# Optimization experiments

Hardware: AMD Instinct MI355X
Metric: run time of the kernel (lower is better)

Reference implementation:

```python
import jax, jax.numpy as jnp
import numpy as np

# ---- static config (from init_kwargs) ----
N = 500_000            # total points
B = 4                  # batch size (lidar frames)
VX, VY, VZ = 0.2, 0.2, 4.0
PC = (0.0, -40.0, -3.0, 70.4, 40.0, 1.0)  # point cloud range
NZ = int((PC[5] - PC[2]) / VZ)   # 1
NY = int((PC[4] - PC[1]) / VY)   # 400
NX = int((PC[3] - PC[0]) / VX)   # 352
CANVAS = B * NZ * NY * NX        # dense voxel canvas (563200)
EPS = 1e-3                       # BN eps
XOFF = VX / 2 + PC[0]
YOFF = VY / 2 + PC[1]
ZOFF = VZ / 2 + PC[2]
C0, C1 = 64, 128                 # feat_channels
CIN = 13                         # 4 + 2(spatial) + 3(cluster) + 3(center) + 1(dist)


def setup_inputs() -> dict:
    key = jax.random.key(0)
    ks = jax.random.split(key, 12)
    # points uniformly in the point-cloud range, plus intensity
    xyz = jax.random.uniform(ks[0], (N, 3), dtype=jnp.float32) \
        * jnp.array([70.4, 80.0, 4.0], jnp.float32) \
        + jnp.array([0.0, -40.0, -3.0], jnp.float32)
    inten = jax.random.uniform(ks[1], (N, 1), dtype=jnp.float32)
    features = jnp.concatenate([xyz, inten], axis=1)  # (N, 4)
    # voxel coords consistent with the points; batch idx sorted so coors[-1,0]==B-1
    bidx = jnp.sort(jax.random.randint(ks[2], (N,), 0, B, dtype=jnp.int32))
    zc = jnp.clip(((xyz[:, 2] - PC[2]) / VZ).astype(jnp.int32), 0, NZ - 1)
    yc = jnp.clip(((xyz[:, 1] - PC[1]) / VY).astype(jnp.int32), 0, NY - 1)
    xc = jnp.clip(((xyz[:, 0] - PC[0]) / VX).astype(jnp.int32), 0, NX - 1)
    coors = jnp.stack([bidx, zc, yc, xc], axis=1)  # (N, 4) [b, z, y, x]
    # VFE weights (Linear bias=False) + BN affine params
    s0 = 1.0 / np.sqrt(CIN)
    s1 = 1.0 / np.sqrt(2 * C0)
    s2 = 1.0 / np.sqrt(C1 + 2)
    W0 = jax.random.uniform(ks[3], (CIN, C0), jnp.float32, -s0, s0)
    g0 = jnp.ones((C0,), jnp.float32)
    b0 = jnp.zeros((C0,), jnp.float32)
    W1 = jax.random.uniform(ks[4], (2 * C0, C1), jnp.float32, -s1, s1)
    g1 = jnp.ones((C1,), jnp.float32)
    b1 = jnp.zeros((C1,), jnp.float32)
    Ws = jax.random.uniform(ks[5], (C1 + 2, C1), jnp.float32, -s2, s2)
    bs = jax.random.uniform(ks[6], (C1,), jnp.float32, -s2, s2)
    return {"features": features, "coors": coors,
            "W0": W0, "g0": g0, "b0": b0,
            "W1": W1, "g1": g1, "b1": b1,
            "Ws": Ws, "bs": bs}


def _bn_relu(x, g, b):
    # BN1d in training mode: batch statistics (biased var), eps=1e-3
    m = jnp.mean(x, axis=0)
    v = jnp.var(x, axis=0)
    return jax.nn.relu((x - m) * jax.lax.rsqrt(v + EPS) * g + b)


def reference(features, coors, W0, g0, b0, W1, g1, b1, Ws, bs):
    xyz = features[:, :3]
    # linear voxel id on the dense canvas: b*Z*Y*X + z*Y*X + y*X + x
    v = ((coors[:, 0] * NZ + coors[:, 1]) * NY + coors[:, 2]) * NX + coors[:, 3]
    v = v.astype(jnp.int32)

    # ---- calculate_spatial_features (unique + index_add -> segment reductions) ----
    counts = jax.ops.segment_sum(jnp.ones((N,), features.dtype), v, CANVAS)
    safe = jnp.maximum(counts, 1.0)                       # clamp(min=1)
    density = safe / (VX * VY * VZ)                       # per-voxel point density
    sum_coords = jax.ops.segment_sum(xyz, v, CANVAS)      # (CANVAS, 3)
    voxel_mean = sum_coords / safe[:, None]
    point_mean = voxel_mean[v]                            # gather back to points
    pdist = jnp.linalg.norm(xyz - point_mean, axis=1)
    mean_dist = (jax.ops.segment_sum(pdist, v, CANVAS) / safe)[v]
    f_spatial = jnp.stack([density[v], mean_dist], axis=1)  # (N, 2)

    # ---- cluster center (avg scatter + gather): same voxel mean ----
    f_cluster = xyz - point_mean                          # (N, 3)

    # ---- voxel center offsets ----
    cf = coors.astype(features.dtype)
    f_center = jnp.stack([
        xyz[:, 0] - (cf[:, 3] * VX + XOFF),
        xyz[:, 1] - (cf[:, 2] * VY + YOFF),
        xyz[:, 2] - (cf[:, 1] * VZ + ZOFF)], axis=1)      # (N, 3)

    # ---- distance ----
    f_dist = jnp.linalg.norm(xyz, axis=1, keepdims=True)  # (N, 1)

    x = jnp.concatenate([features, f_spatial, f_cluster, f_center, f_dist], axis=1)  # (N, 13)

    # ---- VFE layer 0: Linear -> BN -> ReLU, scatter-max, gather, concat ----
    p = _bn_relu(x @ W0, g0, b0)                          # (N, 64)
    vmax = jax.ops.segment_max(p, v, CANVAS)              # (CANVAS, 64), -inf on empty
    x = jnp.concatenate([p, vmax[v]], axis=1)             # (N, 128)

    # ---- VFE layer 1 + feature_scaling ----
    p = _bn_relu(x @ W1, g1, b1)                          # (N, 128)
    p = jax.nn.relu(jnp.concatenate([p, f_spatial], axis=1) @ Ws + bs)  # (N, 128)
    return p  # return_point_feats=True
```

## Files before the change

### kernel.cpp

```cpp
#include <hip/hip_runtime.h>
#include <hip/hip_bf16.h>

#define NZv 1
#define NYv 400
#define NXv 352
#define Bv 4
#define CANVASv (Bv * NZv * NYv * NXv)
#define EPSF 0.001f
#define VXF 0.2f
#define VYF 0.2f
#define VZF 4.0f
#define XOFFv 0.1f
#define YOFFv -39.9f
#define ZOFFv -1.0f

typedef __attribute__((ext_vector_type(8))) short bf16x8;
typedef __attribute__((ext_vector_type(4))) float f32x4;
typedef __attribute__((ext_vector_type(2))) unsigned int u32x2;

__device__ __forceinline__ short f2bf(float f) {
    union { __hip_bfloat16 h; short s; } u;
    u.h = __float2bfloat16(f);
    return u.s;
}
__device__ __forceinline__ float bf2f(short s) {
    return __uint_as_float(((unsigned int)(unsigned short)s) << 16);
}
__device__ __forceinline__ unsigned int pk(float a, float b) {
    return (unsigned int)(unsigned short)f2bf(a) | ((unsigned int)(unsigned short)f2bf(b) << 16);
}

struct MomTab { signed char a[105]; signed char b[105]; };
constexpr MomTab make_momtab() {
    MomTab m{};
    int idx = 0;
    for (int a = 0; a < 14; ++a)
        for (int b = a; b < 14; ++b) { m.a[idx] = (signed char)a; m.b[idx] = (signed char)b; ++idx; }
    return m;
}
constexpr MomTab MT = make_momtab();

__global__ void k_scatter1(const int4* __restrict__ coors, int* __restrict__ vidx,
                           float* __restrict__ counts, int n)
{
    int i = blockIdx.x * blockDim.x + threadIdx.x;
    if (i >= n) return;
    int4 c = coors[i];
    int v = ((c.x * NZv + c.y) * NYv + c.z) * NXv + c.w;
    vidx[i] = v;
    atomicAdd(&counts[v], 1.0f);
}

__global__ __launch_bounds__(1024) void k_scanA(const float* __restrict__ counts,
                                                int* __restrict__ starts, int* __restrict__ bsum)
{
    __shared__ int sdata[1024];
    int t = threadIdx.x;
    int v = blockIdx.x * 1024 + t;
    int c = (int)counts[v];
    sdata[t] = c;
    __syncthreads();
#pragma unroll
    for (int off = 1; off < 1024; off <<= 1) {
        int val = (t >= off) ? sdata[t - off] : 0;
        __syncthreads();
        sdata[t] += val;
        __syncthreads();
    }
    starts[v] = sdata[t] - c;
    if (t == 1023) bsum[blockIdx.x] = sdata[t];
}

__global__ __launch_bounds__(1024) void k_scanBC(const int* __restrict__ bsum,
                                                 int* __restrict__ starts)
{
    __shared__ int red[16];
    int b = blockIdx.x, t = threadIdx.x;
    int v = (t < b) ? bsum[t] : 0;
    for (int m = 1; m < 64; m <<= 1) v += __shfl_xor(v, m);
    int lane = t & 63, w = t >> 6;
    if (lane == 0) red[w] = v;
    __syncthreads();
    if (t == 0) {
        int s = 0;
#pragma unroll
        for (int q = 0; q < 16; ++q) s += red[q];
        red[0] = s;
    }
    __syncthreads();
    starts[b * 1024 + t] += red[0];
}

__global__ void k_perm(const int* __restrict__ vidx, int* __restrict__ starts,
                       int* __restrict__ perm, int n)
{
    int i = blockIdx.x * blockDim.x + threadIdx.x;
    if (i >= n) return;
    int pos = atomicAdd(&starts[vidx[i]], 1);
    perm[pos] = i;
}

__global__ __launch_bounds__(256) void k_seg(const float4* __restrict__ feat,
                                             const int* __restrict__ startsPost,
                                             const int* __restrict__ perm,
                                             float4* __restrict__ vstat, int nvox)
{
    int stride = gridDim.x * blockDim.x;
    for (int v = blockIdx.x * blockDim.x + threadIdx.x; v < nvox; v += stride) {
        int end = startsPost[v];
        int begin = (v > 0) ? startsPost[v - 1] : 0;
        if (begin == end) continue;
        float sx = 0.f, sy = 0.f, sz = 0.f;
        for (int j = begin; j < end; ++j) {
            float4 f = feat[perm[j]];
            sx += f.x; sy += f.y; sz += f.z;
        }
        float inv = 1.0f / (float)(end - begin);
        float mx = sx * inv, my = sy * inv, mz = sz * inv;
        float pd = 0.f;
        for (int j = begin; j < end; ++j) {
            float4 f = feat[perm[j]];
            float dx = f.x - mx, dy = f.y - my, dz = f.z - mz;
            pd += sqrtf(dx * dx + dy * dy + dz * dz);
        }
        vstat[v] = make_float4(mx, my, mz, pd * inv);
    }
}

__global__ __launch_bounds__(256, 1) void k_prexm(const float4* __restrict__ feat,
                       const int4* __restrict__ coors,
                       const int* __restrict__ vidx, const float* __restrict__ counts,
                       const float4* __restrict__ vstat,
                       unsigned int* __restrict__ x, unsigned int* __restrict__ fspc,
                       double* __restrict__ md0, int n)
{
    float acc[105];
#pragma unroll
    for (int e = 0; e < 105; ++e) acc[e] = 0.f;
    int t = threadIdx.x;
    int stride = gridDim.x * blockDim.x;
    for (int i = blockIdx.x * blockDim.x + t; i < n; i += stride) {
        float4 f = feat[i];
        int4 c = coors[i];
        int v = vidx[i];
        float safe = fmaxf(counts[v], 1.0f);
        float4 vs = vstat[v];
        float vals[14];
        vals[0] = f.x; vals[1] = f.y; vals[2] = f.z; vals[3] = f.w;
        vals[4] = safe / 0.16f;
        vals[5] = vs.w;
        vals[6] = f.x - vs.x;
        vals[7] = f.y - vs.y;
        vals[8] = f.z - vs.z;
        vals[9]  = f.x - ((float)c.w * VXF + XOFFv);
        vals[10] = f.y - ((float)c.z * VYF + YOFFv);
        vals[11] = f.z - ((float)c.y * VZF + ZOFFv);
        vals[12] = sqrtf(f.x * f.x + f.y * f.y + f.z * f.z);
        vals[13] = 1.0f;
        unsigned int row[8];
#pragma unroll
        for (int q = 0; q < 6; ++q) row[q] = pk(vals[2 * q], vals[2 * q + 1]);
        row[6] = pk(vals[12], 0.f);
        row[7] = 0u;
        uint4* dst = (uint4*)(x + (size_t)i * 8);
        dst[0] = make_uint4(row[0], row[1], row[2], row[3]);
        dst[1] = make_uint4(row[4], row[5], row[6], row[7]);
        fspc[i] = row[2];
        float qv[14];
#pragma unroll
        for (int k = 0; k < 13; ++k)
            qv[k] = bf2f((short)((k & 1) ? (row[k >> 1] >> 16) : (row[k >> 1] & 0xFFFF)));
        qv[13] = 1.0f;
#pragma unroll
        for (int e = 0; e < 105; ++e)
            acc[e] = fmaf(qv[MT.a[e]], qv[MT.b[e]], acc[e]);
    }
    __shared__ float wacc[4][105];
    int lane = t & 63, wid = t >> 6;
#pragma unroll
    for (int e = 0; e < 105; ++e) {
        float v = acc[e];
        v += __shfl_xor(v, 1);
        v += __shfl_xor(v, 2);
        v += __shfl_xor(v, 4);
        v += __shfl_xor(v, 8);
        v += __shfl_xor(v, 16);
        v += __shfl_xor(v, 32);
        if (lane == 0) wacc[wid][e] = v;
    }
    __syncthreads();
    if (t < 105) {
        double s = (double)wacc[0][t] + (double)wacc[1][t] + (double)wacc[2][t] + (double)wacc[3][t];
        atomicAdd(&md0[t], s);
    }
}

__device__ __forceinline__ int idx14(int a, int b) {
    return a * 14 - a * (a - 1) / 2 + (b - a);
}

__global__ void k_fin0(const double* __restrict__ md0, const float* __restrict__ W0,
                       const float* __restrict__ g0, const float* __restrict__ b0,
                       float* __restrict__ sc0, float* __restrict__ sh0, int n)
{
    __shared__ double mom[105];
    int t = threadIdx.x;
    for (int e = t; e < 105; e += 64) mom[e] = md0[e];
    __syncthreads();
    double nn = (double)n;
    double mu[13];
#pragma unroll
    for (int j = 0; j < 13; ++j) mu[j] = mom[idx14(j, 13)] / nn;
    double wc[13];
#pragma unroll
    for (int j = 0; j < 13; ++j) wc[j] = (double)W0[j * 64 + t];
    double meanc = 0.0, var = 0.0;
#pragma unroll
    for (int j = 0; j < 13; ++j) {
        meanc += mu[j] * wc[j];
        for (int k = 0; k < 13; ++k) {
            int a = j < k ? j : k, b = j < k ? k : j;
            double cov = mom[idx14(a, b)] / nn - mu[j] * mu[k];
            var += cov * wc[j] * wc[k];
        }
    }
    float scale = g0[t] * rsqrtf((float)var + EPSF);
    sc0[t] = scale;
    sh0[t] = b0[t] - (float)meanc * scale;
}

__global__ __launch_bounds__(256) void k_vmaxv(const unsigned int* __restrict__ x,
    const float* __restrict__ W0, const float* __restrict__ sc0, const float* __restrict__ sh0,
    const int* __restrict__ startsPost, const int* __restrict__ perm,
    unsigned int* __restrict__ p0, unsigned int* __restrict__ vmaxb, int nvox)
{
    int t = threadIdx.x, lane = t & 63, wid = t >> 6;
    float wcol[13];
#pragma unroll
    for (int k = 0; k < 13; ++k) wcol[k] = W0[k * 64 + lane];
    float sc = sc0[lane], sh = sh0[lane];
    int nw = gridDim.x * 4;
    for (int v = blockIdx.x * 4 + wid; v < nvox; v += nw) {
        int end = startsPost[v];
        int begin = (v > 0) ? startsPost[v - 1] : 0;
        if (begin == end) continue;
        float m = 0.f;
        for (int j = begin; j < end; ++j) {
            int i = perm[j];
            const uint4* xr = (const uint4*)(x + (size_t)i * 8);
            uint4 r0 = xr[0], r1 = xr[1];
            unsigned int rw[8] = {r0.x, r0.y, r0.z, r0.w, r1.x, r1.y, r1.z, r1.w};
            float acc = 0.f;
#pragma unroll
            for (int k = 0; k < 13; ++k) {
                float xv = bf2f((short)((k & 1) ? (rw[k >> 1] >> 16) : (rw[k >> 1] & 0xFFFF)));
                acc = fmaf(xv, wcol[k], acc);
            }
            float pv = fmaxf(fmaf(acc, sc, sh), 0.f);
            float pn = __shfl_xor(pv, 1);
            if ((lane & 1) == 0)
                p0[(size_t)i * 32 + (lane >> 1)] = pk(pv, pn);
            m = fmaxf(m, pv);
        }
        float mn = __shfl_xor(m, 1);
        if ((lane & 1) == 0)
            vmaxb[(size_t)v * 32 + (lane >> 1)] = pk(m, mn);
    }
}

#define G1_SW1 0
#define G1_SX  32768
#define G1_ST  65536
#define G1_LDS (65536 + 8192)

__global__ __launch_bounds__(512) void k_gstat(const unsigned int* __restrict__ p0,
    const unsigned int* __restrict__ vmaxb, const int* __restrict__ vidx,
    const float* __restrict__ W1,
    double* __restrict__ s1d, double* __restrict__ sq1d, int n, int ntiles)
{
    extern __shared__ char lds[];
    char* sW1 = lds + G1_SW1;
    char* sx  = lds + G1_SX;
    int t = threadIdx.x, lane = t & 63, w = t >> 6;
    int pl = lane & 15, qd = lane >> 4;

#pragma unroll
    for (int it = 0; it < 8; ++it) {
        int e = (it * 512 + t) * 4;
        float4 wv = *(const float4*)(W1 + e);
        int k = e >> 7, c0 = e & 127;
        float wa[4] = {wv.x, wv.y, wv.z, wv.w};
#pragma unroll
        for (int qq = 0; qq < 4; ++qq) {
            int c = c0 + qq;
            *(short*)(sW1 + c * 256 + ((k * 2) ^ ((c & 7) << 4))) = f2bf(wa[qq]);
        }
    }
    __syncthreads();

    float st_s[8][4], st_q[8][4];
#pragma unroll
    for (int cb = 0; cb < 8; ++cb)
#pragma unroll
        for (int jj = 0; jj < 4; ++jj) { st_s[cb][jj] = 0.f; st_q[cb][jj] = 0.f; }

    unsigned int szr = (unsigned int)(pl & 7) << 4;
    int rb_ = w * 16 + pl;
    for (int tile = blockIdx.x; tile < ntiles; tile += gridDim.x) {
        int base = tile * 128;
        {
            int p = t >> 2, s = t & 3;
            int i = base + p;
            char* rowp = sx + p * 256;
            unsigned int sz = (unsigned int)(p & 7) << 4;
            uint4 d0, d1, d2, d3;
            if (i < n) {
                const uint4* src = (s < 2)
                    ? (const uint4*)(p0 + (size_t)i * 32 + s * 16)
                    : (const uint4*)(vmaxb + (size_t)vidx[i] * 32 + (s - 2) * 16);
                d0 = src[0]; d1 = src[1]; d2 = src[2]; d3 = src[3];
            } else {
                d0 = d1 = d2 = d3 = make_uint4(0u, 0u, 0u, 0u);
            }
            int k2 = s * 64;
            *(uint4*)(rowp + ((k2 +  0) ^ sz)) = d0;
            *(uint4*)(rowp + ((k2 + 16) ^ sz)) = d1;
            *(uint4*)(rowp + ((k2 + 32) ^ sz)) = d2;
            *(uint4*)(rowp + ((k2 + 48) ^ sz)) = d3;
        }
        __syncthreads();
        f32x4 acc[8];
#pragma unroll
        for (int cb = 0; cb < 8; ++cb) acc[cb] = (f32x4){0.f, 0.f, 0.f, 0.f};
#pragma unroll
        for (int kc = 0; kc < 4; ++kc) {
            int ko2 = kc * 64 + qd * 16;
            bf16x8 b = *(bf16x8*)(sx + rb_ * 256 + (ko2 ^ szr));
#pragma unroll
            for (int cb = 0; cb < 8; ++cb) {
                int ra_ = cb * 16 + pl;
                bf16x8 a = *(bf16x8*)(sW1 + ra_ * 256 + (ko2 ^ szr));
                acc[cb] = __builtin_amdgcn_mfma_f32_16x16x32_bf16(a, b, acc[cb], 0, 0, 0);
            }
        }
        int pt = base + rb_;
        if (pt < n) {
#pragma unroll
            for (int cb = 0; cb < 8; ++cb)
#pragma unroll
                for (int jj = 0; jj < 4; ++jj) {
                    float av = acc[cb][jj];
                    st_s[cb][jj] += av;
                    st_q[cb][jj] = fmaf(av, av, st_q[cb][jj]);
                }
        }
        __syncthreads();
    }
    float* ssum = (float*)(lds + G1_ST);
    float* ssq  = ssum + 8 * 128;
#pragma unroll
    for (int cb = 0; cb < 8; ++cb)
#pragma unroll
        for (int jj = 0; jj < 4; ++jj) {
            float sv = st_s[cb][jj], qv = st_q[cb][jj];
            sv += __shfl_xor(sv, 1); qv += __shfl_xor(qv, 1);
            sv += __shfl_xor(sv, 2); qv += __shfl_xor(qv, 2);
            sv += __shfl_xor(sv, 4); qv += __shfl_xor(qv, 4);
            sv += __shfl_xor(sv, 8); qv += __shfl_xor(qv, 8);
            if (pl == 0) {
                int ch = cb * 16 + qd * 4 + jj;
                ssum[w * 128 + ch] = sv;
                ssq[w * 128 + ch] = qv;
            }
        }
    __syncthreads();
    if (t < 128) {
        float s = 0.f, q = 0.f;
#pragma unroll
        for (int ww = 0; ww < 8; ++ww) { s += ssum[ww * 128 + t]; q += ssq[ww * 128 + t]; }
        atomicAdd(&s1d[t], (double)s);
        atomicAdd(&sq1d[t], (double)q);
    }
}

__global__ void k_fin1s(const double* __restrict__ s1d, const double* __restrict__ sq1d,
                        const float* __restrict__ g1, const float* __restrict__ b1,
                        float* __restrict__ sc1, float* __restrict__ sh1, int n)
{
    int c = threadIdx.x;
    double mean = s1d[c] / (double)n;
    double var = sq1d[c] / (double)n - mean * mean;
    float scale = g1[c] * rsqrtf((float)var + EPSF);
    sc1[c] = scale;
    sh1[c] = b1[c] - (float)mean * scale;
}

#define F3_SW1 0
#define F3_SWS 32768
#define F3_SX  (32768 + 49152)
#define F3_SCL (32768 + 49152 + 49152)
#define F3_LDS (F3_SCL + 1536)

__global__ __launch_bounds__(512) void k_fused3(const unsigned int* __restrict__ p0,
    const unsigned int* __restrict__ vmaxb, const int* __restrict__ vidx,
    const unsigned int* __restrict__ fspc,
    const float* __restrict__ W1, const float* __restrict__ Wsp, const float* __restrict__ bsp,
    const float* __restrict__ sc1, const float* __restrict__ sh1,
    float* __restrict__ out, int n, int ntiles)
{
    extern __shared__ char lds[];
    char* sW1 = lds + F3_SW1;
    char* sWs = lds + F3_SWS;
    char* sx  = lds + F3_SX;
    float* ssc = (float*)(lds + F3_SCL);
    float* ssh = ssc + 128;
    float* sbs = ssh + 128;
    int t = threadIdx.x, lane = t & 63, w = t >> 6;
    int pl = lane & 15, qd = lane >> 4;

#pragma unroll
    for (int it = 0; it < 8; ++it) {
        int e = (it * 512 + t) * 4;
        float4 wv = *(const float4*)(W1 + e);
        int k = e >> 7, c0 = e & 127;
        float wa[4] = {wv.x, wv.y, wv.z, wv.w};
#pragma unroll
        for (int qq = 0; qq < 4; ++qq) {
            int c = c0 + qq;
            *(short*)(sW1 + c * 256 + ((k * 2) ^ ((c & 7) << 4))) = f2bf(wa[qq]);
        }
    }
    for (int it = 0; it < 9; ++it) {
        int e = (it * 512 + t) * 4;
        if (e < 16640) {
            float4 wv = *(const float4*)(Wsp + e);
            int k = e >> 7, c0 = e & 127;
            float wa[4] = {wv.x, wv.y, wv.z, wv.w};
#pragma unroll
            for (int qq = 0; qq < 4; ++qq) {
                int c = c0 + qq;
                *(short*)(sWs + c * 384 + ((k * 2) ^ ((c & 7) << 4))) = f2bf(wa[qq]);
            }
        }
    }
    for (int e = t; e < 128 * 15; e += 512) {
        int r = e / 15, qq = e - r * 15;
        int k2 = 260 + 4 * qq;
        *(unsigned int*)(sWs + r * 384 + (k2 ^ ((r & 7) << 4))) = 0u;
        *(unsigned int*)(sx  + r * 384 + (k2 ^ ((r & 7) << 4))) = 0u;
    }
    if (t < 128) { ssc[t] = sc1[t]; ssh[t] = sh1[t]; sbs[t] = bsp[t]; }
    __syncthreads();

    unsigned int szr = (unsigned int)(pl & 7) << 4;
    int rb_ = w * 16 + pl;
    for (int tile = blockIdx.x; tile < ntiles; tile += gridDim.x) {
        int base = tile * 128;
        {
            int p = t >> 2, s = t & 3;
            int i = base + p;
            char* rowp = sx + p * 384;
            unsigned int sz = (unsigned int)(p & 7) << 4;
            uint4 d0, d1, d2, d3;
            if (i < n) {
                const uint4* src = (s < 2)
                    ? (const uint4*)(p0 + (size_t)i * 32 + s * 16)
                    : (const uint4*)(vmaxb + (size_t)vidx[i] * 32 + (s - 2) * 16);
                d0 = src[0]; d1 = src[1]; d2 = src[2]; d3 = src[3];
            } else {
                d0 = d1 = d2 = d3 = make_uint4(0u, 0u, 0u, 0u);
            }
            int k2 = s * 64;
            *(uint4*)(rowp + ((k2 +  0) ^ sz)) = d0;
            *(uint4*)(rowp + ((k2 + 16) ^ sz)) = d1;
            *(uint4*)(rowp + ((k2 + 32) ^ sz)) = d2;
            *(uint4*)(rowp + ((k2 + 48) ^ sz)) = d3;
        }
        __syncthreads();
        f32x4 acc1[8];
#pragma unroll
        for (int cb = 0; cb < 8; ++cb) acc1[cb] = (f32x4){0.f, 0.f, 0.f, 0.f};
#pragma unroll
        for (int kc = 0; kc < 4; ++kc) {
            int ko2 = kc * 64 + qd * 16;
            bf16x8 b = *(bf16x8*)(sx + rb_ * 384 + (ko2 ^ szr));
#pragma unroll
            for (int cb = 0; cb < 8; ++cb) {
                int ra_ = cb * 16 + pl;
                bf16x8 a = *(bf16x8*)(sW1 + ra_ * 256 + (ko2 ^ szr));
                acc1[cb] = __builtin_amdgcn_mfma_f32_16x16x32_bf16(a, b, acc1[cb], 0, 0, 0);
            }
        }
#pragma unroll
        for (int cb = 0; cb < 8; ++cb) {
            int ch0 = cb * 16 + qd * 4;
            float v0 = fmaxf(fmaf(acc1[cb][0], ssc[ch0 + 0], ssh[ch0 + 0]), 0.f);
            float v1 = fmaxf(fmaf(acc1[cb][1], ssc[ch0 + 1], ssh[ch0 + 1]), 0.f);
            float v2 = fmaxf(fmaf(acc1[cb][2], ssc[ch0 + 2], ssh[ch0 + 2]), 0.f);
            float v3 = fmaxf(fmaf(acc1[cb][3], ssc[ch0 + 3], ssh[ch0 + 3]), 0.f);
            u32x2 o;
            o.x = pk(v0, v1);
            o.y = pk(v2, v3);
            *(u32x2*)(sx + rb_ * 384 + ((unsigned int)(cb * 32 + qd * 8) ^ szr)) = o;
        }
        if (qd == 0) {
            int i = base + rb_; if (i >= n) i = n - 1;
            unsigned int fs = fspc[i];
            *(unsigned int*)(sx + rb_ * 384 + (256u ^ szr)) = fs;
        }
        f32x4 acc2[8];
#pragma unroll
        for (int cb = 0; cb < 8; ++cb) acc2[cb] = (f32x4){0.f, 0.f, 0.f, 0.f};
#pragma unroll
        for (int kc = 0; kc < 5; ++kc) {
            int ko2 = kc * 64 + qd * 16;
            bf16x8 b = *(bf16x8*)(sx + rb_ * 384 + (ko2 ^ szr));
#pragma unroll
            for (int cb = 0; cb < 8; ++cb) {
                int ra_ = cb * 16 + pl;
                bf16x8 a = *(bf16x8*)(sWs + ra_ * 384 + (ko2 ^ szr));
                acc2[cb] = __builtin_amdgcn_mfma_f32_16x16x32_bf16(a, b, acc2[cb], 0, 0, 0);
            }
        }
        int pt = base + rb_;
        if (pt < n) {
            float* orow = out + (size_t)pt * 128 + qd * 4;
#pragma unroll
            for (int cb = 0; cb < 8; ++cb) {
                float4 bb = *(float4*)(sbs + cb * 16 + qd * 4);
                f32x4 o;
                o[0] = fmaxf(acc2[cb][0] + bb.x, 0.f);
                o[1] = fmaxf(acc2[cb][1] + bb.y, 0.f);
                o[2] = fmaxf(acc2[cb][2] + bb.z, 0.f);
                o[3] = fmaxf(acc2[cb][3] + bb.w, 0.f);
                __builtin_nontemporal_store(o, (f32x4*)(orow + cb * 16));
            }
        }
        __syncthreads();
    }
}

extern "C" void kernel_launch(void* const* d_in, const int* in_sizes, int n_in,
                              void* d_out, int out_size, void* d_ws, size_t ws_size,
                              hipStream_t stream)
{
    const float* feat = (const float*)d_in[0];
    const int*   coor = (const int*)d_in[1];
    const float* W0   = (const float*)d_in[2];
    const float* g0   = (const float*)d_in[3];
    const float* b0   = (const float*)d_in[4];
    const float* W1   = (const float*)d_in[5];
    const float* g1   = (const float*)d_in[6];
    const float* b1   = (const float*)d_in[7];
    const float* Wsp  = (const float*)d_in[8];
    const float* bsp  = (const float*)d_in[9];
    float* outp = (float*)d_out;

    int n = in_sizes[0] / 4;
    size_t npad = ((size_t)n + 127) & ~127ULL;

    char* ws = (char*)d_ws;
    size_t off = 0;
    auto alloc = [&](size_t bytes) { char* p = ws + off; off = (off + bytes + 255) & ~255ULL; return p; };
    int*          vidx   = (int*)alloc(npad * 4);
    float*        counts = (float*)alloc((size_t)CANVASv * 4);
    double*       md0    = (double*)alloc(105 * 8 + 256 * 8);
    double*       s1d    = (double*)((char*)md0 + 105 * 8);
    double*       sq1d   = s1d + 128;
    float4*       vstat  = (float4*)alloc((size_t)CANVASv * 16);
    unsigned int* x      = (unsigned int*)alloc(npad * 32);
    unsigned int* fspc   = (unsigned int*)alloc(npad * 4);
    unsigned int* p0     = (unsigned int*)alloc(npad * 128);
    unsigned int* vmaxb  = (unsigned int*)alloc((size_t)CANVASv * 128);
    int*          starts = (int*)alloc((size_t)CANVASv * 4);
    int*          perm   = (int*)alloc(npad * 4);
    int*          bsum   = (int*)alloc(1024 * 4);
    float*        sc0    = (float*)alloc(64 * 4);
    float*        sh0    = (float*)alloc(64 * 4);
    float*        sc1    = (float*)alloc(128 * 4);
    float*        sh1    = (float*)alloc(128 * 4);
    if (off > ws_size) return;

    hipMemsetAsync(counts, 0, (size_t)CANVASv * 4 + 105 * 8 + 256 * 8, stream);

    int blocksN = (n + 255) / 256;
    k_scatter1<<<blocksN, 256, 0, stream>>>((const int4*)coor, vidx, counts, n);

    k_scanA<<<CANVASv / 1024, 1024, 0, stream>>>(counts, starts, bsum);
    k_scanBC<<<CANVASv / 1024, 1024, 0, stream>>>(bsum, starts);
    k_perm<<<blocksN, 256, 0, stream>>>(vidx, starts, perm, n);

    k_seg<<<1024, 256, 0, stream>>>((const float4*)feat, starts, perm, vstat, CANVASv);

    k_prexm<<<512, 256, 0, stream>>>((const float4*)feat, (const int4*)coor, vidx, counts, vstat, x, fspc, md0, n);
    k_fin0<<<1, 64, 0, stream>>>(md0, W0, g0, b0, sc0, sh0, n);

    k_vmaxv<<<2048, 256, 0, stream>>>(x, W0, sc0, sh0, starts, perm, p0, vmaxb, CANVASv);

    int ntiles = (n + 127) / 128;
    hipFuncSetAttribute((const void*)k_gstat, hipFuncAttributeMaxDynamicSharedMemorySize, G1_LDS);
    k_gstat<<<512, 512, G1_LDS, stream>>>(p0, vmaxb, vidx, W1, s1d, sq1d, n, ntiles);
    k_fin1s<<<1, 128, 0, stream>>>(s1d, sq1d, g1, b1, sc1, sh1, n);

    hipFuncSetAttribute((const void*)k_fused3, hipFuncAttributeMaxDynamicSharedMemorySize, F3_LDS);
    k_fused3<<<256, 512, F3_LDS, stream>>>(p0, vmaxb, vidx, fspc, W1, Wsp, bsp, sc1, sh1, outp, n, ntiles);
}
```

Baseline: 409.3 us.

## Split fused VFE-1 kernel channel work across two wave halves with 1024-thread blocks

Doubles the block to 1024 threads. Each group of 8 waves now computes half of the 128 output channels for the same 128-point tile, so each wave holds 4 accumulators instead of 8. The aim is to cut per-wave register pressure and serial MFMA chains, and to get more waves in flight for latency hiding. The cost is an extra block-wide barrier between the two GEMMs, needed because layer-1 outputs are now written by both halves, plus redundant B-operand LDS reads in each half.

```diff
diff --git a/kernel.cpp b/kernel.cpp
--- a/kernel.cpp
+++ b/kernel.cpp
@@ -401,7 +401,7 @@
 #define F3_SCL (32768 + 49152 + 49152)
 #define F3_LDS (F3_SCL + 1536)
 
-__global__ __launch_bounds__(512) void k_fused3(const unsigned int* __restrict__ p0,
+__global__ __launch_bounds__(1024) void k_fused4(const unsigned int* __restrict__ p0,
     const unsigned int* __restrict__ vmaxb, const int* __restrict__ vidx,
     const unsigned int* __restrict__ fspc,
     const float* __restrict__ W1, const float* __restrict__ Wsp, const float* __restrict__ bsp,
@@ -417,10 +417,13 @@
     float* sbs = ssh + 128;
     int t = threadIdx.x, lane = t & 63, w = t >> 6;
     int pl = lane & 15, qd = lane >> 4;
-
-#pragma unroll
-    for (int it = 0; it < 8; ++it) {
-        int e = (it * 512 + t) * 4;
+    int h = w >> 3;
+    int wr = w & 7;
+    int cbase = h * 4;
+
+#pragma unroll
+    for (int it = 0; it < 4; ++it) {
+        int e = (it * 1024 + t) * 4;
         float4 wv = *(const float4*)(W1 + e);
         int k = e >> 7, c0 = e & 127;
         float wa[4] = {wv.x, wv.y, wv.z, wv.w};
@@ -430,8 +433,8 @@
             *(short*)(sW1 + c * 256 + ((k * 2) ^ ((c & 7) << 4))) = f2bf(wa[qq]);
         }
     }
-    for (int it = 0; it < 9; ++it) {
-        int e = (it * 512 + t) * 4;
+    for (int it = 0; it < 5; ++it) {
+        int e = (it * 1024 + t) * 4;
         if (e < 16640) {
             float4 wv = *(const float4*)(Wsp + e);
             int k = e >> 7, c0 = e & 127;
@@ -443,7 +446,7 @@
             }
         }
     }
-    for (int e = t; e < 128 * 15; e += 512) {
+    for (int e = t; e < 128 * 15; e += 1024) {
         int r = e / 15, qq = e - r * 15;
         int k2 = 260 + 4 * qq;
         *(unsigned int*)(sWs + r * 384 + (k2 ^ ((r & 7) << 4))) = 0u;
@@ -453,86 +456,87 @@
     __syncthreads();
 
     unsigned int szr = (unsigned int)(pl & 7) << 4;
-    int rb_ = w * 16 + pl;
+    int rb_ = wr * 16 + pl;
     for (int tile = blockIdx.x; tile < ntiles; tile += gridDim.x) {
         int base = tile * 128;
         {
-            int p = t >> 2, s = t & 3;
+            int p = t >> 3, s = t & 7;
             int i = base + p;
             char* rowp = sx + p * 384;
             unsigned int sz = (unsigned int)(p & 7) << 4;
-            uint4 d0, d1, d2, d3;
+            uint4 d0, d1;
             if (i < n) {
-                const uint4* src = (s < 2)
-                    ? (const uint4*)(p0 + (size_t)i * 32 + s * 16)
-                    : (const uint4*)(vmaxb + (size_t)vidx[i] * 32 + (s - 2) * 16);
-                d0 = src[0]; d1 = src[1]; d2 = src[2]; d3 = src[3];
+                const uint4* src = (s < 4)
+                    ? (const uint4*)(p0 + (size_t)i * 32 + s * 8)
+                    : (const uint4*)(vmaxb + (size_t)vidx[i] * 32 + (s - 4) * 8);
+                d0 = src[0]; d1 = src[1];
             } else {
-                d0 = d1 = d2 = d3 = make_uint4(0u, 0u, 0u, 0u);
-            }
-            int k2 = s * 64;
+                d0 = d1 = make_uint4(0u, 0u, 0u, 0u);
+            }
+            int k2 = s * 32;
             *(uint4*)(rowp + ((k2 +  0) ^ sz)) = d0;
             *(uint4*)(rowp + ((k2 + 16) ^ sz)) = d1;
-            *(uint4*)(rowp + ((k2 + 32) ^ sz)) = d2;
-            *(uint4*)(rowp + ((k2 + 48) ^ sz)) = d3;
         }
         __syncthreads();
-        f32x4 acc1[8];
-#pragma unroll
-        for (int cb = 0; cb < 8; ++cb) acc1[cb] = (f32x4){0.f, 0.f, 0.f, 0.f};
+        f32x4 acc1[4];
+#pragma unroll
+        for (int c4 = 0; c4 < 4; ++c4) acc1[c4] = (f32x4){0.f, 0.f, 0.f, 0.f};
 #pragma unroll
         for (int kc = 0; kc < 4; ++kc) {
             int ko2 = kc * 64 + qd * 16;
             bf16x8 b = *(bf16x8*)(sx + rb_ * 384 + (ko2 ^ szr));
 #pragma unroll
-            for (int cb = 0; cb < 8; ++cb) {
-                int ra_ = cb * 16 + pl;
+            for (int c4 = 0; c4 < 4; ++c4) {
+                int ra_ = (cbase + c4) * 16 + pl;
                 bf16x8 a = *(bf16x8*)(sW1 + ra_ * 256 + (ko2 ^ szr));
-                acc1[cb] = __builtin_amdgcn_mfma_f32_16x16x32_bf16(a, b, acc1[cb], 0, 0, 0);
-            }
-        }
-#pragma unroll
-        for (int cb = 0; cb < 8; ++cb) {
+                acc1[c4] = __builtin_amdgcn_mfma_f32_16x16x32_bf16(a, b, acc1[c4], 0, 0, 0);
+            }
+        }
+#pragma unroll
+        for (int c4 = 0; c4 < 4; ++c4) {
+            int cb = cbase + c4;
             int ch0 = cb * 16 + qd * 4;
-            float v0 = fmaxf(fmaf(acc1[cb][0], ssc[ch0 + 0], ssh[ch0 + 0]), 0.f);
-            float v1 = fmaxf(fmaf(acc1[cb][1], ssc[ch0 + 1], ssh[ch0 + 1]), 0.f);
-            float v2 = fmaxf(fmaf(acc1[cb][2], ssc[ch0 + 2], ssh[ch0 + 2]), 0.f);
-            float v3 = fmaxf(fmaf(acc1[cb][3], ssc[ch0 + 3], ssh[ch0 + 3]), 0.f);
+            float v0 = fmaxf(fmaf(acc1[c4][0], ssc[ch0 + 0], ssh[ch0 + 0]), 0.f);
+            float v1 = fmaxf(fmaf(acc1[c4][1], ssc[ch0 + 1], ssh[ch0 + 1]), 0.f);
+            float v2 = fmaxf(fmaf(acc1[c4][2], ssc[ch0 + 2], ssh[ch0 + 2]), 0.f);
+            float v3 = fmaxf(fmaf(acc1[c4][3], ssc[ch0 + 3], ssh[ch0 + 3]), 0.f);
             u32x2 o;
             o.x = pk(v0, v1);
             o.y = pk(v2, v3);
             *(u32x2*)(sx + rb_ * 384 + ((unsigned int)(cb * 32 + qd * 8) ^ szr)) = o;
         }
-        if (qd == 0) {
+        if (h == 0 && qd == 0) {
             int i = base + rb_; if (i >= n) i = n - 1;
             unsigned int fs = fspc[i];
             *(unsigned int*)(sx + rb_ * 384 + (256u ^ szr)) = fs;
         }
-        f32x4 acc2[8];
-#pragma unroll
-        for (int cb = 0; cb < 8; ++cb) acc2[cb] = (f32x4){0.f, 0.f, 0.f, 0.f};
+        __syncthreads();
+        f32x4 acc2[4];
+#pragma unroll
+        for (int c4 = 0; c4 < 4; ++c4) acc2[c4] = (f32x4){0.f, 0.f, 0.f, 0.f};
 #pragma unroll
         for (int kc = 0; kc < 5; ++kc) {
             int ko2 = kc * 64 + qd * 16;
             bf16x8 b = *(bf16x8*)(sx + rb_ * 384 + (ko2 ^ szr));
 #pragma unroll
-            for (int cb = 0; cb < 8; ++cb) {
-                int ra_ = cb * 16 + pl;
+            for (int c4 = 0; c4 < 4; ++c4) {
+                int ra_ = (cbase + c4) * 16 + pl;
                 bf16x8 a = *(bf16x8*)(sWs + ra_ * 384 + (ko2 ^ szr));
-                acc2[cb] = __builtin_amdgcn_mfma_f32_16x16x32_bf16(a, b, acc2[cb], 0, 0, 0);
+                acc2[c4] = __builtin_amdgcn_mfma_f32_16x16x32_bf16(a, b, acc2[c4], 0, 0, 0);
             }
         }
         int pt = base + rb_;
         if (pt < n) {
             float* orow = out + (size_t)pt * 128 + qd * 4;
 #pragma unroll
-            for (int cb = 0; cb < 8; ++cb) {
+            for (int c4 = 0; c4 < 4; ++c4) {
+                int cb = cbase + c4;
                 float4 bb = *(float4*)(sbs + cb * 16 + qd * 4);
                 f32x4 o;
-                o[0] = fmaxf(acc2[cb][0] + bb.x, 0.f);
-                o[1] = fmaxf(acc2[cb][1] + bb.y, 0.f);
-                o[2] = fmaxf(acc2[cb][2] + bb.z, 0.f);
-                o[3] = fmaxf(acc2[cb][3] + bb.w, 0.f);
+                o[0] = fmaxf(acc2[c4][0] + bb.x, 0.f);
+                o[1] = fmaxf(acc2[c4][1] + bb.y, 0.f);
+                o[2] = fmaxf(acc2[c4][2] + bb.z, 0.f);
+                o[3] = fmaxf(acc2[c4][3] + bb.w, 0.f);
                 __builtin_nontemporal_store(o, (f32x4*)(orow + cb * 16));
             }
         }
@@ -602,6 +606,6 @@
     k_gstat<<<512, 512, G1_LDS, stream>>>(p0, vmaxb, vidx, W1, s1d, sq1d, n, ntiles);
     k_fin1s<<<1, 128, 0, stream>>>(s1d, sq1d, g1, b1, sc1, sh1, n);
 
-    hipFuncSetAttribute((const void*)k_fused3, hipFuncAttributeMaxDynamicSharedMemorySize, F3_LDS);
-    k_fused3<<<256, 512, F3_LDS, stream>>>(p0, vmaxb, vidx, fspc, W1, Wsp, bsp, sc1, sh1, outp, n, ntiles);
-}
+    hipFuncSetAttribute((const void*)k_fused4, hipFuncAttributeMaxDynamicSharedMemorySize, F3_LDS);
+    k_fused4<<<256, 1024, F3_LDS, stream>>>(p0, vmaxb, vidx, fspc, W1, Wsp, bsp, sc1, sh1, outp, n, ntiles);
+}
```

New measurement: 415.4 us. Within noise of the previous version (+1.5%).
